# Performance work log

Measured on AMD Instinct MI355X. Metric: run time of the kernel, lower is better.

Reference implementation:

```python
import jax, jax.numpy as jnp
import numpy as np

B, N, D, H = 2, 192, 256, 8
DH = D // H
SCALE = 1.0 / float(np.sqrt(DH))


def setup_inputs() -> dict:
    key = jax.random.key(0)
    ks = jax.random.split(key, 20)
    def w(k, shape, s=0.02):
        return jax.random.normal(k, shape, dtype=jnp.float32) * s
    inp = {}
    inp['x'] = jax.random.normal(ks[0], (B, N, D), dtype=jnp.float32)
    inp['e'] = jax.random.normal(ks[1], (B, N, N, D), dtype=jnp.float32)
    for name in ['ln_x', 'ln_e', 'ln_x2', 'ln_e2']:
        inp[name + '_g'] = jnp.ones((D,), jnp.float32)
        inp[name + '_b'] = jnp.zeros((D,), jnp.float32)
    # per-head stacked projection weights: [H, D, DH]
    for i, n in enumerate(['Wq_en', 'Wk_en', 'Wv_en', 'Wq_ne', 'Wk_ne', 'Wv_ne']):
        inp[n] = w(ks[2 + i], (H, D, DH))
        inp['b' + n[1:]] = jnp.zeros((H, DH), jnp.float32)
    inp['WOx_w'] = w(ks[10], (D, D)); inp['WOx_b'] = jnp.zeros((D,), jnp.float32)
    inp['WOe_w'] = w(ks[11], (D, D)); inp['WOe_b'] = jnp.zeros((D,), jnp.float32)
    inp['mlpx_w1'] = w(ks[12], (4 * D, D)); inp['mlpx_b1'] = jnp.zeros((4 * D,), jnp.float32)
    inp['mlpx_w2'] = w(ks[13], (D, 4 * D)); inp['mlpx_b2'] = jnp.zeros((D,), jnp.float32)
    inp['mlpe_w1'] = w(ks[14], (4 * D, D)); inp['mlpe_b1'] = jnp.zeros((4 * D,), jnp.float32)
    inp['mlpe_w2'] = w(ks[15], (D, 4 * D)); inp['mlpe_b2'] = jnp.zeros((D,), jnp.float32)
    return inp


def layer_norm(v, g, b, eps=1e-5):
    m = jnp.mean(v, axis=-1, keepdims=True)
    var = jnp.mean((v - m) ** 2, axis=-1, keepdims=True)
    return (v - m) * jax.lax.rsqrt(var + eps) * g + b


def reference(x, e, ln_x_g, ln_x_b, ln_e_g, ln_e_b, ln_x2_g, ln_x2_b, ln_e2_g, ln_e2_b,
              Wq_en, bq_en, Wk_en, bk_en, Wv_en, bv_en,
              Wq_ne, bq_ne, Wk_ne, bk_ne, Wv_ne, bv_ne,
              WOx_w, WOx_b, WOe_w, WOe_b,
              mlpx_w1, mlpx_b1, mlpx_w2, mlpx_b2,
              mlpe_w1, mlpe_b1, mlpe_w2, mlpe_b2):
    b_, n_, d_ = x.shape
    xn = layer_norm(x, ln_x_g, ln_x_b)
    en = layer_norm(e, ln_e_g, ln_e_b)

    # --- edge-to-node cross attention (node i attends over its edges (i, j)) ---
    Q = jnp.einsum('bnd,hde->bnhe', xn, Wq_en) + bq_en          # [B,N,H,DH]
    K = jnp.einsum('bijd,hde->bijhe', en, Wk_en) + bk_en        # [B,N,N,H,DH]
    V = jnp.einsum('bijd,hde->bijhe', en, Wv_en) + bv_en
    s = jnp.einsum('bihe,bijhe->bijh', Q, K) * SCALE            # [B,N,N,H]
    a = jax.nn.softmax(s, axis=2)
    x_heads = jnp.einsum('bijh,bijhe->bihe', a, V)              # [B,N,H,DH]
    x_mha = x_heads.reshape(b_, n_, d_) @ WOx_w.T + WOx_b

    # --- node-to-edge cross attention (edge (i,j) attends over endpoints i, j) ---
    Qe = jnp.einsum('bijd,hde->bijhe', en, Wq_ne) + bq_ne       # [B,N,N,H,DH]
    Kx = jnp.einsum('bnd,hde->bnhe', xn, Wk_ne) + bk_ne         # [B,N,H,DH]
    Vx = jnp.einsum('bnd,hde->bnhe', xn, Wv_ne) + bv_ne
    si = jnp.einsum('bijhe,bihe->bijh', Qe, Kx) * SCALE
    sj = jnp.einsum('bijhe,bjhe->bijh', Qe, Kx) * SCALE
    m = jnp.maximum(si, sj)
    ei = jnp.exp(si - m)
    ej = jnp.exp(sj - m)
    den = ei + ej
    ai = (ei / den)[..., None]                                   # [B,N,N,H,1]
    aj = (ej / den)[..., None]
    e_heads = ai * Vx[:, :, None] + aj * Vx[:, None, :]          # [B,N,N,H,DH]
    e_mha = e_heads.reshape(b_, n_, n_, d_) @ WOe_w.T + WOe_b

    # --- residuals + MLPs ---
    x_out = xn + x_mha
    hx = layer_norm(x_out, ln_x2_g, ln_x2_b)
    hx = jax.nn.leaky_relu(hx @ mlpx_w1.T + mlpx_b1, 0.01) @ mlpx_w2.T + mlpx_b2
    x_out = x_out + hx

    e_out = en + e_mha
    he = layer_norm(e_out, ln_e2_g, ln_e2_b)
    he = jax.nn.leaky_relu(he @ mlpe_w1.T + mlpe_b1, 0.01) @ mlpe_w2.T + mlpe_b2
    e_out = e_out + he
    return (x_out, e_out)
```

## Files before the change

### kernel.cpp

```cpp
#include <hip/hip_runtime.h>
#include <hip/hip_bf16.h>
#include <math.h>

#define BB 2
#define NN 192
#define DD 256
#define HH 8
#define DHH 32
#define SCALE 0.17677669529663687f
#define SJ 4
#define NTILE (BB * NN * 6)

typedef __attribute__((ext_vector_type(8))) short short8;
typedef __attribute__((ext_vector_type(4))) float f32x4;


__device__ __forceinline__ float red32(float v) {
    v += __shfl_xor(v, 16);
    v += __shfl_xor(v, 8);
    v += __shfl_xor(v, 4);
    v += __shfl_xor(v, 2);
    v += __shfl_xor(v, 1);
    return v;
}

__device__ __forceinline__ unsigned short f2bf(float f) {
    unsigned int u = __builtin_bit_cast(unsigned int, f);
    u += 0x7FFFu + ((u >> 16) & 1u);
    return (unsigned short)(u >> 16);
}

__device__ __forceinline__ float bf2f(unsigned short u) {
    unsigned int v = ((unsigned int)u) << 16;
    return __builtin_bit_cast(float, v);
}

__device__ __forceinline__ void ln8(float (*xs)[DD], const float* __restrict__ g,
                                    const float* __restrict__ b,
                                    float* mred, float* rred) {
    int t = threadIdx.x;
    int r = t >> 5, l = t & 31;
    float s = 0.f, s2 = 0.f;
#pragma unroll
    for (int u = 0; u < 8; u++) {
        float v = xs[r][l + 32 * u];
        s += v; s2 += v * v;
    }
    s = red32(s); s2 = red32(s2);
    if (l == 0) {
        float mean = s * (1.f / 256.f);
        float var  = s2 * (1.f / 256.f) - mean * mean;
        mred[r] = mean;
        rred[r] = rsqrtf(var + 1e-5f);
    }
    __syncthreads();
    float gt = g[t], bt = b[t];
#pragma unroll
    for (int rr = 0; rr < 8; rr++) {
        float v = xs[rr][t];
        xs[rr][t] = (v - mred[rr]) * rred[rr] * gt + bt;
    }
    __syncthreads();
}

__device__ __forceinline__ void gemm256f8(const unsigned short (*A)[264],
                                          const unsigned short* __restrict__ Wf,
                                          int w, int lane, int fr, int fq,
                                          f32x4 acc[2][2]) {
#pragma unroll
    for (int m = 0; m < 2; m++)
#pragma unroll
        for (int nt = 0; nt < 2; nt++) acc[m][nt] = (f32x4){0.f, 0.f, 0.f, 0.f};
    short8 nb[2];
#pragma unroll
    for (int nt = 0; nt < 2; nt++)
        nb[nt] = *(const short8*)(Wf + (((size_t)(w * 2 + nt) * 8 + 0) * 64 + lane) * 8);
#pragma unroll
    for (int k = 0; k < 8; k++) {
        short8 cb[2];
#pragma unroll
        for (int nt = 0; nt < 2; nt++) cb[nt] = nb[nt];
        if (k < 7) {
#pragma unroll
            for (int nt = 0; nt < 2; nt++)
                nb[nt] = *(const short8*)(Wf + (((size_t)(w * 2 + nt) * 8 + k + 1) * 64 + lane) * 8);
        }
        short8 a0 = *(const short8*)&A[fr][k * 32 + fq * 8];
        short8 a1 = *(const short8*)&A[16 + fr][k * 32 + fq * 8];
#pragma unroll
        for (int nt = 0; nt < 2; nt++) {
            acc[0][nt] = __builtin_amdgcn_mfma_f32_16x16x32_bf16(a0, cb[nt], acc[0][nt], 0, 0, 0);
            acc[1][nt] = __builtin_amdgcn_mfma_f32_16x16x32_bf16(a1, cb[nt], acc[1][nt], 0, 0, 0);
        }
    }
}

__global__ void k_node_prep(const float* __restrict__ x,
                            const float* __restrict__ lnxg, const float* __restrict__ lnxb,
                            const float* __restrict__ Wq, const float* __restrict__ bq,
                            const float* __restrict__ Wk, const float* __restrict__ bk,
                            const float* __restrict__ Wv, const float* __restrict__ bv,
                            float* __restrict__ xn, float* __restrict__ Qb,
                            float* __restrict__ Kx, float* __restrict__ Vx) {
    __shared__ float xs[8][DD];
    __shared__ float mred[8], rred[8];
    int t = threadIdx.x;
    int r0 = blockIdx.x * 8;
    for (int r = 0; r < 8; r++) xs[r][t] = x[(r0 + r) * DD + t];
    __syncthreads();
    ln8(xs, lnxg, lnxb, mred, rred);
    for (int r = 0; r < 8; r++) xn[(r0 + r) * DD + t] = xs[r][t];
    int h = t >> 5, d_ = t & 31;
    const float* wq = Wq + h * DD * DHH + d_;
    const float* wk = Wk + h * DD * DHH + d_;
    const float* wv = Wv + h * DD * DHH + d_;
    float aq[8] = {0}, ak[8] = {0}, av[8] = {0};
    for (int k = 0; k < DD; k++) {
        float w1 = wq[k * DHH], w2 = wk[k * DHH], w3 = wv[k * DHH];
#pragma unroll
        for (int r = 0; r < 8; r++) {
            float e = xs[r][k];
            aq[r] += e * w1; ak[r] += e * w2; av[r] += e * w3;
        }
    }
    float bqt = bq[t], bkt = bk[t], bvt = bv[t];
    for (int r = 0; r < 8; r++) {
        Qb[(r0 + r) * DD + t] = aq[r] + bqt;
        Kx[(r0 + r) * DD + t] = ak[r] + bkt;
        Vx[(r0 + r) * DD + t] = av[r] + bvt;
    }
}

__global__ void k_cvt_all(const float* __restrict__ w1, const float* __restrict__ w2,
                          const float* __restrict__ WOe,
                          const float* __restrict__ Wq, const float* __restrict__ Wk,
                          const float* __restrict__ Wv,
                          unsigned short* __restrict__ w1f, unsigned short* __restrict__ w2f,
                          unsigned short* __restrict__ WOef,
                          unsigned short* __restrict__ Wqf, unsigned short* __restrict__ Wkf,
                          unsigned short* __restrict__ Wvf) {
    int bid = blockIdx.x, t = threadIdx.x;
    short8 out;
    if (bid < 128) {
        int fi = bid * 256 + t;
        int l = fi & 63, g = fi >> 6;
        int fr = l & 15, fq = l >> 4;
        int tau = g >> 3, kap = g & 7;
        const float* src = w1 + (size_t)(tau * 16 + fr) * 256 + kap * 32 + fq * 8;
#pragma unroll
        for (int u = 0; u < 8; u++) out[u] = (short)f2bf(src[u]);
        *(short8*)(w1f + (size_t)fi * 8) = out;
    } else if (bid < 256) {
        int fi = (bid - 128) * 256 + t;
        int l = fi & 63, g = fi >> 6;
        int fr = l & 15, fq = l >> 4;
        int tau = g >> 5, kap = g & 31;
        const float* src = w2 + (size_t)(tau * 16 + fr) * 1024 + kap * 32 + fq * 8;
#pragma unroll
        for (int u = 0; u < 8; u++) out[u] = (short)f2bf(src[u]);
        *(short8*)(w2f + (size_t)fi * 8) = out;
    } else if (bid < 288) {
        int fi = (bid - 256) * 256 + t;
        int l = fi & 63, g = fi >> 6;
        int fr = l & 15, fq = l >> 4;
        int tau = g >> 3, kap = g & 7;
        const float* src = WOe + (size_t)(tau * 16 + fr) * 256 + kap * 32 + fq * 8;
#pragma unroll
        for (int u = 0; u < 8; u++) out[u] = (short)f2bf(src[u]);
        *(short8*)(WOef + (size_t)fi * 8) = out;
    } else {
        int which = (bid - 288) >> 5;
        int fi = ((bid - 288) & 31) * 256 + t;
        int l = fi & 63, g = fi >> 6;
        int fr = l & 15, fq = l >> 4;
        int tau = g >> 3, kap = g & 7;
        int n = tau * 16 + fr;
        int k0 = kap * 32 + fq * 8;
        const float* src = which == 0 ? Wq : which == 1 ? Wk : Wv;
        const float* s2 = src + (size_t)(n >> 5) * 8192 + (n & 31);
#pragma unroll
        for (int u = 0; u < 8; u++) out[u] = (short)f2bf(s2[(size_t)(k0 + u) * 32]);
        unsigned short* dst = which == 0 ? Wqf : which == 1 ? Wkf : Wvf;
        *(short8*)(dst + (size_t)fi * 8) = out;
    }
}

__global__ __launch_bounds__(512, 2) void k_n2e_fused(
    const float* __restrict__ e,
    const float* __restrict__ lneg, const float* __restrict__ lneb,
    const unsigned short* __restrict__ Wqf, const float* __restrict__ bq,
    const unsigned short* __restrict__ Wkf, const float* __restrict__ bk,
    const unsigned short* __restrict__ Wvf, const float* __restrict__ bv,
    const float* __restrict__ Kx, const float* __restrict__ Vx,
    const unsigned short* __restrict__ WOef, const float* __restrict__ WOb,
    const float* __restrict__ ln2g, const float* __restrict__ ln2b,
    const unsigned short* __restrict__ w1f, const float* __restrict__ b1,
    const unsigned short* __restrict__ w2f, const float* __restrict__ b2,
    float* __restrict__ oute, unsigned short* __restrict__ Kb,
    unsigned short* __restrict__ Vb) {
    __shared__ unsigned short a_bf[32][264];
    __shared__ unsigned short p_bf[32][264];
    __shared__ float KxiS[DD], VxiS[DD];
    __shared__ float mrow[32], rrow[32];
    __shared__ float sW[32][8], s2W[32][8];
    __shared__ float m2s[32], r2s[32];
    int t = threadIdx.x, lane = t & 63, w = t >> 6;
    int fr = lane & 15, fq = lane >> 4;
    int blk = blockIdx.x;
    int b   = blk / (NN * 6);
    int rem = blk % (NN * 6);
    int i   = rem / 6;
    int j0  = (rem % 6) * 32;
    int node = b * NN + i;
    size_t ebase = ((size_t)node * NN + j0) * DD;

    {
        int r = t >> 4, sub = t & 15;
        const float4* src4 = (const float4*)(e + ebase + (size_t)r * DD + sub * 16);
        float vals[16];
        float s = 0.f, s2 = 0.f;
#pragma unroll
        for (int u = 0; u < 4; u++) {
            float4 v = src4[u];
            vals[4 * u + 0] = v.x; vals[4 * u + 1] = v.y;
            vals[4 * u + 2] = v.z; vals[4 * u + 3] = v.w;
            s += v.x + v.y + v.z + v.w;
            s2 += v.x * v.x + v.y * v.y + v.z * v.z + v.w * v.w;
        }
        s += __shfl_xor(s, 8); s2 += __shfl_xor(s2, 8);
        s += __shfl_xor(s, 4); s2 += __shfl_xor(s2, 4);
        s += __shfl_xor(s, 2); s2 += __shfl_xor(s2, 2);
        s += __shfl_xor(s, 1); s2 += __shfl_xor(s2, 1);
        float mean = s * (1.f / 256.f);
        float rstd = rsqrtf(s2 * (1.f / 256.f) - mean * mean + 1e-5f);
        if (sub == 0) { mrow[r] = mean; rrow[r] = rstd; }
#pragma unroll
        for (int u = 0; u < 16; u += 2) {
            int col = sub * 16 + u;
            float n0 = (vals[u]     - mean) * rstd * lneg[col]     + lneb[col];
            float n1 = (vals[u + 1] - mean) * rstd * lneg[col + 1] + lneb[col + 1];
            unsigned int pk = (unsigned int)f2bf(n0) | ((unsigned int)f2bf(n1) << 16);
            *(unsigned int*)&a_bf[r][col] = pk;
        }
    }
    if (t < DD) {
        KxiS[t] = Kx[node * DD + t];
        VxiS[t] = Vx[node * DD + t];
    }
    __syncthreads();

    const int nw = w * 32;

    f32x4 accQ[2][2];
    gemm256f8(a_bf, Wqf, w, lane, fr, fq, accQ);
    {
        float bqv[2];
#pragma unroll
        for (int nt = 0; nt < 2; nt++) bqv[nt] = bq[nw + nt * 16 + fr];
#pragma unroll
        for (int m = 0; m < 2; m++)
#pragma unroll
            for (int nt = 0; nt < 2; nt++)
#pragma unroll
                for (int j = 0; j < 4; j++) accQ[m][nt][j] += bqv[nt];
    }

    {
        f32x4 accK[2][2];
        gemm256f8(a_bf, Wkf, w, lane, fr, fq, accK);
#pragma unroll
        for (int nt = 0; nt < 2; nt++) {
            float bb = bk[nw + nt * 16 + fr];
#pragma unroll
            for (int m = 0; m < 2; m++)
#pragma unroll
                for (int j = 0; j < 4; j++)
                    p_bf[m * 16 + fq * 4 + j][nw + nt * 16 + fr] = f2bf(accK[m][nt][j] + bb);
        }
    }
    __syncthreads();
#pragma unroll
    for (int rp = 0; rp < 2; rp++) {
        int r = rp * 16 + (t >> 5);
        int c = (t & 31) * 8;
        short8 v = *(const short8*)&p_bf[r][c];
        *(short8*)(Kb + ebase + (size_t)r * DD + c) = v;
    }
    __syncthreads();

    {
        f32x4 accV[2][2];
        gemm256f8(a_bf, Wvf, w, lane, fr, fq, accV);
#pragma unroll
        for (int nt = 0; nt < 2; nt++) {
            float bb = bv[nw + nt * 16 + fr];
#pragma unroll
            for (int m = 0; m < 2; m++)
#pragma unroll
                for (int j = 0; j < 4; j++)
                    p_bf[m * 16 + fq * 4 + j][nw + nt * 16 + fr] = f2bf(accV[m][nt][j] + bb);
        }
    }
    __syncthreads();
#pragma unroll
    for (int rp = 0; rp < 2; rp++) {
        int r = rp * 16 + (t >> 5);
        int c = (t & 31) * 8;
        short8 v = *(const short8*)&p_bf[r][c];
        *(short8*)(Vb + ebase + (size_t)r * DD + c) = v;
    }
    __syncthreads();

    float KxiL[2], VxiL[2];
#pragma unroll
    for (int nt = 0; nt < 2; nt++) {
        KxiL[nt] = KxiS[nw + nt * 16 + fr];
        VxiL[nt] = VxiS[nw + nt * 16 + fr];
    }
    float ai[2][4], aj[2][4];
    {
        float Kxj[2][2][4];
#pragma unroll
        for (int m = 0; m < 2; m++)
#pragma unroll
            for (int nt = 0; nt < 2; nt++)
#pragma unroll
                for (int j = 0; j < 4; j++) {
                    int row = m * 16 + fq * 4 + j;
                    Kxj[m][nt][j] = Kx[(size_t)(b * NN + j0 + row) * DD + nw + nt * 16 + fr];
                }
#pragma unroll
        for (int m = 0; m < 2; m++)
#pragma unroll
            for (int j = 0; j < 4; j++) {
                float p = accQ[m][0][j] * KxiL[0] + accQ[m][1][j] * KxiL[1];
                float q = accQ[m][0][j] * Kxj[m][0][j] + accQ[m][1][j] * Kxj[m][1][j];
#pragma unroll
                for (int mk = 1; mk <= 8; mk <<= 1) {
                    p += __shfl_xor(p, mk);
                    q += __shfl_xor(q, mk);
                }
                p *= SCALE; q *= SCALE;
                float mx = fmaxf(p, q);
                float ei = __expf(p - mx), ej = __expf(q - mx);
                float inv = 1.f / (ei + ej);
                ai[m][j] = ei * inv; aj[m][j] = ej * inv;
            }
    }
    {
        float Vxj[2][2][4];
#pragma unroll
        for (int m = 0; m < 2; m++)
#pragma unroll
            for (int nt = 0; nt < 2; nt++)
#pragma unroll
                for (int j = 0; j < 4; j++) {
                    int row = m * 16 + fq * 4 + j;
                    Vxj[m][nt][j] = Vx[(size_t)(b * NN + j0 + row) * DD + nw + nt * 16 + fr];
                }
#pragma unroll
        for (int m = 0; m < 2; m++)
#pragma unroll
            for (int nt = 0; nt < 2; nt++)
#pragma unroll
                for (int j = 0; j < 4; j++) {
                    float v = ai[m][j] * VxiL[nt] + aj[m][j] * Vxj[m][nt][j];
                    p_bf[m * 16 + fq * 4 + j][nw + nt * 16 + fr] = f2bf(v);
                }
    }
    __syncthreads();

    f32x4 accO[2][2];
    gemm256f8(p_bf, WOef, w, lane, fr, fq, accO);

    float epre[2][2][4];
#pragma unroll
    for (int nt = 0; nt < 2; nt++) {
        int col = nw + nt * 16 + fr;
        float bo = WOb[col];
        float gc = lneg[col], bc = lneb[col];
#pragma unroll
        for (int m = 0; m < 2; m++)
#pragma unroll
            for (int j = 0; j < 4; j++) {
                int row = m * 16 + fq * 4 + j;
                float ev = e[ebase + (size_t)row * DD + col];
                float resid = (ev - mrow[row]) * rrow[row] * gc + bc;
                epre[m][nt][j] = resid + accO[m][nt][j] + bo;
            }
    }

#pragma unroll
    for (int m = 0; m < 2; m++)
#pragma unroll
        for (int j = 0; j < 4; j++) {
            float s  = epre[m][0][j] + epre[m][1][j];
            float s2 = epre[m][0][j] * epre[m][0][j] + epre[m][1][j] * epre[m][1][j];
#pragma unroll
            for (int mk = 1; mk <= 8; mk <<= 1) {
                s += __shfl_xor(s, mk);
                s2 += __shfl_xor(s2, mk);
            }
            if (fr == 0) {
                int row = m * 16 + fq * 4 + j;
                sW[row][w] = s;
                s2W[row][w] = s2;
            }
        }
    __syncthreads();
    if (t < 32) {
        float S = 0.f, S2 = 0.f;
#pragma unroll
        for (int ww = 0; ww < 8; ww++) { S += sW[t][ww]; S2 += s2W[t][ww]; }
        float mean = S * (1.f / 256.f);
        float var  = S2 * (1.f / 256.f) - mean * mean;
        m2s[t] = mean;
        r2s[t] = rsqrtf(var + 1e-5f);
    }
    __syncthreads();

#pragma unroll
    for (int nt = 0; nt < 2; nt++) {
        int col = nw + nt * 16 + fr;
        float g2 = ln2g[col], b2c = ln2b[col];
#pragma unroll
        for (int m = 0; m < 2; m++)
#pragma unroll
            for (int j = 0; j < 4; j++) {
                int row = m * 16 + fq * 4 + j;
                p_bf[row][col] = f2bf((epre[m][nt][j] - m2s[row]) * r2s[row] * g2 + b2c);
            }
    }
    __syncthreads();

#define B1ADDR(c, nt, k) (w1f + (((size_t)((c) * 16 + w * 2 + (nt)) * 8 + (k)) * 64 + lane) * 8)
#define B2ADDR(nt, c, k) (w2f + (((size_t)(w * 2 + (nt)) * 32 + (c) * 8 + (k)) * 64 + lane) * 8)
    f32x4 accM[2][2];
#pragma unroll
    for (int m = 0; m < 2; m++)
#pragma unroll
        for (int nt = 0; nt < 2; nt++) accM[m][nt] = (f32x4){0.f, 0.f, 0.f, 0.f};

    for (int c = 0; c < 4; c++) {
        f32x4 acc1[2][2];
#pragma unroll
        for (int m = 0; m < 2; m++)
#pragma unroll
            for (int nt = 0; nt < 2; nt++) acc1[m][nt] = (f32x4){0.f, 0.f, 0.f, 0.f};
        {
            short8 nb[2];
#pragma unroll
            for (int nt = 0; nt < 2; nt++) nb[nt] = *(const short8*)B1ADDR(c, nt, 0);
#pragma unroll
            for (int k = 0; k < 8; k++) {
                short8 cb[2];
#pragma unroll
                for (int nt = 0; nt < 2; nt++) cb[nt] = nb[nt];
                if (k < 7) {
#pragma unroll
                    for (int nt = 0; nt < 2; nt++) nb[nt] = *(const short8*)B1ADDR(c, nt, k + 1);
                }
                short8 a0 = *(const short8*)&p_bf[fr][k * 32 + fq * 8];
                short8 a1 = *(const short8*)&p_bf[16 + fr][k * 32 + fq * 8];
#pragma unroll
                for (int nt = 0; nt < 2; nt++) {
                    acc1[0][nt] = __builtin_amdgcn_mfma_f32_16x16x32_bf16(a0, cb[nt], acc1[0][nt], 0, 0, 0);
                    acc1[1][nt] = __builtin_amdgcn_mfma_f32_16x16x32_bf16(a1, cb[nt], acc1[1][nt], 0, 0, 0);
                }
            }
        }
#pragma unroll
        for (int nt = 0; nt < 2; nt++) {
            int ncol = nw + nt * 16 + fr;
            float bias = b1[c * 256 + ncol];
#pragma unroll
            for (int m = 0; m < 2; m++)
#pragma unroll
                for (int j = 0; j < 4; j++) {
                    float v = acc1[m][nt][j] + bias;
                    v = v > 0.f ? v : 0.01f * v;
                    a_bf[m * 16 + fq * 4 + j][ncol] = f2bf(v);
                }
        }
        __syncthreads();
        {
            short8 nb[2];
#pragma unroll
            for (int nt = 0; nt < 2; nt++) nb[nt] = *(const short8*)B2ADDR(nt, c, 0);
#pragma unroll
            for (int k = 0; k < 8; k++) {
                short8 cb[2];
#pragma unroll
                for (int nt = 0; nt < 2; nt++) cb[nt] = nb[nt];
                if (k < 7) {
#pragma unroll
                    for (int nt = 0; nt < 2; nt++) nb[nt] = *(const short8*)B2ADDR(nt, c, k + 1);
                }
                short8 h0 = *(const short8*)&a_bf[fr][k * 32 + fq * 8];
                short8 h1 = *(const short8*)&a_bf[16 + fr][k * 32 + fq * 8];
#pragma unroll
                for (int nt = 0; nt < 2; nt++) {
                    accM[0][nt] = __builtin_amdgcn_mfma_f32_16x16x32_bf16(h0, cb[nt], accM[0][nt], 0, 0, 0);
                    accM[1][nt] = __builtin_amdgcn_mfma_f32_16x16x32_bf16(h1, cb[nt], accM[1][nt], 0, 0, 0);
                }
            }
        }
        __syncthreads();
    }
#undef B1ADDR
#undef B2ADDR

#pragma unroll
    for (int nt = 0; nt < 2; nt++) {
        int col = nw + nt * 16 + fr;
        float bias = b2[col];
#pragma unroll
        for (int m = 0; m < 2; m++)
#pragma unroll
            for (int j = 0; j < 4; j++) {
                int row = m * 16 + fq * 4 + j;
                oute[ebase + (size_t)row * DD + col] = epre[m][nt][j] + accM[m][nt][j] + bias;
            }
    }
}

__global__ void k_e2n_lite(const unsigned short* __restrict__ Kb,
                           const unsigned short* __restrict__ Vb,
                           const float* __restrict__ Qb,
                           float* __restrict__ accP, float* __restrict__ mP,
                           float* __restrict__ lP) {
    __shared__ float accS[8][DD];
    __shared__ float mS[8][HH], lS[8][HH];
    int t = threadIdx.x;
    int s = blockIdx.x & (SJ - 1);
    int row = blockIdx.x >> 2;
    int g = t >> 5;
    int d0 = (t & 31) * 8;
    float qv[8];
    {
        const float4* q4 = (const float4*)(Qb + (size_t)row * DD + d0);
        float4 a = q4[0], b4 = q4[1];
        qv[0] = a.x; qv[1] = a.y; qv[2] = a.z; qv[3] = a.w;
        qv[4] = b4.x; qv[5] = b4.y; qv[6] = b4.z; qv[7] = b4.w;
    }
    float m_s = -1e30f, l_s = 0.f;
    float acc[8];
#pragma unroll
    for (int u = 0; u < 8; u++) acc[u] = 0.f;
    size_t base = (size_t)row * NN * DD;
    for (int it = 0; it < NN / SJ / 8; it++) {
        int j = s * (NN / SJ) + it * 8 + g;
        short8 kv = *(const short8*)(Kb + base + (size_t)j * DD + d0);
        short8 vv = *(const short8*)(Vb + base + (size_t)j * DD + d0);
        float part = 0.f;
#pragma unroll
        for (int u = 0; u < 8; u++) part += qv[u] * bf2f((unsigned short)kv[u]);
        part += __shfl_xor(part, 1);
        part += __shfl_xor(part, 2);
        float sc = part * SCALE;
        float mn = fmaxf(m_s, sc);
        float c = __expf(m_s - mn);
        float p = __expf(sc - mn);
        l_s = l_s * c + p;
#pragma unroll
        for (int u = 0; u < 8; u++) acc[u] = acc[u] * c + p * bf2f((unsigned short)vv[u]);
        m_s = mn;
    }
#pragma unroll
    for (int u = 0; u < 8; u++) accS[g][d0 + u] = acc[u];
    if ((t & 3) == 0) {
        int h = (t & 31) >> 2;
        mS[g][h] = m_s;
        lS[g][h] = l_s;
    }
    __syncthreads();
    int H = t >> 5;
    float mm = -1e30f;
#pragma unroll
    for (int g2 = 0; g2 < 8; g2++) mm = fmaxf(mm, mS[g2][H]);
    float ll = 0.f, aa = 0.f;
#pragma unroll
    for (int g2 = 0; g2 < 8; g2++) {
        float c = __expf(mS[g2][H] - mm);
        ll += lS[g2][H] * c;
        aa += accS[g2][t] * c;
    }
    accP[((size_t)s * BB * NN + row) * DD + t] = aa;
    if ((t & 31) == 0) {
        mP[(s * BB * NN + row) * HH + H] = mm;
        lP[(s * BB * NN + row) * HH + H] = ll;
    }
}

__global__ void k_e2n_merge(const float* __restrict__ accP, const float* __restrict__ mP,
                            const float* __restrict__ lP, float* __restrict__ xh) {
    int t = threadIdx.x, row = blockIdx.x, h = t >> 5;
    float m = -1e30f;
    for (int s = 0; s < SJ; s++) m = fmaxf(m, mP[(s * BB * NN + row) * HH + h]);
    float num = 0.f, den = 0.f;
    for (int s = 0; s < SJ; s++) {
        float c = __expf(mP[(s * BB * NN + row) * HH + h] - m);
        num += accP[((size_t)s * BB * NN + row) * DD + t] * c;
        den += lP[(s * BB * NN + row) * HH + h] * c;
    }
    xh[row * DD + t] = num / den;
}

__global__ void k_x_epi(const float* __restrict__ xh, const float* __restrict__ xn,
                        const float* __restrict__ WO, const float* __restrict__ WOb,
                        const float* __restrict__ ln2g, const float* __restrict__ ln2b,
                        const float* __restrict__ w1, const float* __restrict__ b1,
                        const float* __restrict__ w2, const float* __restrict__ b2,
                        float* __restrict__ outx) {
    __shared__ float hsrc[8][DD];
    __shared__ float xs[8][DD];
    __shared__ float ls[8][DD];
    __shared__ float hh[8][1024];
    __shared__ float mred[8], rred[8];
    int t = threadIdx.x;
    int r0 = blockIdx.x * 8;
    for (int r = 0; r < 8; r++) hsrc[r][t] = xh[(r0 + r) * DD + t];
    __syncthreads();
    float acc[8] = {0};
    const float* wrow = WO + (size_t)t * DD;
    for (int k = 0; k < DD; k++) {
        float w = wrow[k];
#pragma unroll
        for (int r = 0; r < 8; r++) acc[r] += hsrc[r][k] * w;
    }
    float wob = WOb[t];
    for (int r = 0; r < 8; r++) {
        float v = xn[(r0 + r) * DD + t] + acc[r] + wob;
        xs[r][t] = v;
        ls[r][t] = v;
    }
    __syncthreads();
    ln8(ls, ln2g, ln2b, mred, rred);
    for (int p = 0; p < 4; p++) {
        int q = t + p * 256;
        float a2[8] = {0};
        const float* w1r = w1 + (size_t)q * DD;
        for (int k = 0; k < DD; k++) {
            float w = w1r[k];
#pragma unroll
            for (int r = 0; r < 8; r++) a2[r] += ls[r][k] * w;
        }
        float b1q = b1[q];
        for (int r = 0; r < 8; r++) {
            float v = a2[r] + b1q;
            hh[r][q] = v > 0.f ? v : 0.01f * v;
        }
    }
    __syncthreads();
    float a3[8] = {0};
    const float* w2r = w2 + (size_t)t * 1024;
    for (int q = 0; q < 1024; q++) {
        float w = w2r[q];
#pragma unroll
        for (int r = 0; r < 8; r++) a3[r] += hh[r][q] * w;
    }
    float b2t = b2[t];
    for (int r = 0; r < 8; r++)
        outx[(r0 + r) * DD + t] = xs[r][t] + a3[r] + b2t;
}

__global__ void k_e2n_attn(const float* __restrict__ e,
                           const float* __restrict__ lneg, const float* __restrict__ lneb,
                           const float* __restrict__ Wk, const float* __restrict__ bk,
                           const float* __restrict__ Wv, const float* __restrict__ bv,
                           const float* __restrict__ Qb,
                           float* __restrict__ accP, float* __restrict__ mP,
                           float* __restrict__ lP) {
    __shared__ float es[8][DD];
    __shared__ float mred[8], rred[8];
    int t = threadIdx.x;
    int s = blockIdx.x & (SJ - 1);
    int row = blockIdx.x >> 2;
    int h = t >> 5, d_ = t & 31;
    float qt = Qb[row * DD + t];
    float m_s = -1e30f, l_s = 0.f, acc = 0.f;
    const float* wk = Wk + h * DD * DHH + d_;
    const float* wv = Wv + h * DD * DHH + d_;
    float bkt = bk[t], bvt = bv[t];
    for (int j0 = s * (NN / SJ); j0 < (s + 1) * (NN / SJ); j0 += 8) {
        for (int r = 0; r < 8; r++)
            es[r][t] = e[((size_t)row * NN + j0 + r) * DD + t];
        __syncthreads();
        ln8(es, lneg, lneb, mred, rred);
        float aK[8] = {0}, aV[8] = {0};
        for (int k = 0; k < DD; k++) {
            float w1 = wk[k * DHH], w2 = wv[k * DHH];
#pragma unroll
            for (int r = 0; r < 8; r++) {
                float ev = es[r][k];
                aK[r] += ev * w1; aV[r] += ev * w2;
            }
        }
#pragma unroll
        for (int r = 0; r < 8; r++) {
            float sc = red32(qt * (aK[r] + bkt)) * SCALE;
            float vn = aV[r] + bvt;
            float mn = fmaxf(m_s, sc);
            float c = __expf(m_s - mn);
            float p = __expf(sc - mn);
            l_s = l_s * c + p;
            acc = acc * c + p * vn;
            m_s = mn;
        }
        __syncthreads();
    }
    accP[((size_t)s * BB * NN + row) * DD + t] = acc;
    if (d_ == 0) {
        mP[(s * BB * NN + row) * HH + h] = m_s;
        lP[(s * BB * NN + row) * HH + h] = l_s;
    }
}

__global__ void k_n2e(const float* __restrict__ e,
                      const float* __restrict__ lneg, const float* __restrict__ lneb,
                      const float* __restrict__ Wq, const float* __restrict__ bq,
                      const float* __restrict__ Kx, const float* __restrict__ Vx,
                      const float* __restrict__ WO, const float* __restrict__ WOb,
                      float* __restrict__ oute) {
    __shared__ float es[8][DD];
    __shared__ float hs[8][DD];
    __shared__ float mred[8], rred[8];
    int t = threadIdx.x, h = t >> 5, d_ = t & 31;
    int blk = blockIdx.x;
    int b = blk / (NN * (NN / 8));
    int rem = blk % (NN * (NN / 8));
    int i = rem / (NN / 8);
    int j0 = (rem % (NN / 8)) * 8;
    size_t ebase = ((size_t)(b * NN + i) * NN + j0) * DD;
    for (int r = 0; r < 8; r++) es[r][t] = e[ebase + (size_t)r * DD + t];
    __syncthreads();
    ln8(es, lneg, lneb, mred, rred);
    float aQ[8] = {0};
    const float* wq = Wq + h * DD * DHH + d_;
    for (int k = 0; k < DD; k++) {
        float w = wq[k * DHH];
#pragma unroll
        for (int r = 0; r < 8; r++) aQ[r] += es[r][k] * w;
    }
    float bqt = bq[t];
    float kxi = Kx[(b * NN + i) * DD + t];
    float vxi = Vx[(b * NN + i) * DD + t];
#pragma unroll
    for (int r = 0; r < 8; r++) {
        float qe = aQ[r] + bqt;
        float si = red32(qe * kxi) * SCALE;
        float kxj = Kx[(b * NN + j0 + r) * DD + t];
        float sj = red32(qe * kxj) * SCALE;
        float mx = fmaxf(si, sj);
        float ei = __expf(si - mx), ej = __expf(sj - mx);
        float inv = 1.f / (ei + ej);
        float vxj = Vx[(b * NN + j0 + r) * DD + t];
        hs[r][t] = (ei * inv) * vxi + (ej * inv) * vxj;
    }
    __syncthreads();
    float aO[8] = {0};
    const float* wrow = WO + (size_t)t * DD;
    for (int k = 0; k < DD; k++) {
        float w = wrow[k];
#pragma unroll
        for (int r = 0; r < 8; r++) aO[r] += hs[r][k] * w;
    }
    float wob = WOb[t];
    for (int r = 0; r < 8; r++)
        oute[ebase + (size_t)r * DD + t] = es[r][t] + aO[r] + wob;
}

__global__ void k_cvt_w_fb(const float* __restrict__ w1, const float* __restrict__ w2,
                           unsigned short* __restrict__ w1b, unsigned short* __restrict__ w2b) {
    int i = blockIdx.x * 256 + threadIdx.x;
    w1b[i] = f2bf(w1[i]);
    w2b[i] = f2bf(w2[i]);
}

__global__ void k_e_mlp_f32(float* __restrict__ oute,
                            const float* __restrict__ ln2g, const float* __restrict__ ln2b,
                            const float* __restrict__ w1, const float* __restrict__ b1,
                            const float* __restrict__ w2, const float* __restrict__ b2) {
    __shared__ float xs[8][DD];
    __shared__ float ls[8][DD];
    __shared__ float hh[8][1024];
    __shared__ float mred[8], rred[8];
    int t = threadIdx.x;
    size_t r0 = (size_t)blockIdx.x * 8;
    for (int r = 0; r < 8; r++) {
        float v = oute[(r0 + r) * DD + t];
        xs[r][t] = v;
        ls[r][t] = v;
    }
    __syncthreads();
    ln8(ls, ln2g, ln2b, mred, rred);
    for (int p = 0; p < 4; p++) {
        int q = t + p * 256;
        float a2[8] = {0};
        const float* w1r = w1 + (size_t)q * DD;
        for (int k = 0; k < DD; k++) {
            float w = w1r[k];
#pragma unroll
            for (int r = 0; r < 8; r++) a2[r] += ls[r][k] * w;
        }
        float b1q = b1[q];
        for (int r = 0; r < 8; r++) {
            float v = a2[r] + b1q;
            hh[r][q] = v > 0.f ? v : 0.01f * v;
        }
    }
    __syncthreads();
    float a3[8] = {0};
    const float* w2r = w2 + (size_t)t * 1024;
    for (int q = 0; q < 1024; q++) {
        float w = w2r[q];
#pragma unroll
        for (int r = 0; r < 8; r++) a3[r] += hh[r][q] * w;
    }
    float b2t = b2[t];
    for (int r = 0; r < 8; r++)
        oute[(r0 + r) * DD + t] = xs[r][t] + a3[r] + b2t;
}

extern "C" void kernel_launch(void* const* d_in, const int* in_sizes, int n_in,
                              void* d_out, int out_size, void* d_ws, size_t ws_size,
                              hipStream_t stream) {
    (void)in_sizes; (void)n_in; (void)out_size;
    const float* x      = (const float*)d_in[0];
    const float* e      = (const float*)d_in[1];
    const float* ln_x_g = (const float*)d_in[2];
    const float* ln_x_b = (const float*)d_in[3];
    const float* ln_e_g = (const float*)d_in[4];
    const float* ln_e_b = (const float*)d_in[5];
    const float* ln_x2_g = (const float*)d_in[6];
    const float* ln_x2_b = (const float*)d_in[7];
    const float* ln_e2_g = (const float*)d_in[8];
    const float* ln_e2_b = (const float*)d_in[9];
    const float* Wq_en = (const float*)d_in[10];
    const float* bq_en = (const float*)d_in[11];
    const float* Wk_en = (const float*)d_in[12];
    const float* bk_en = (const float*)d_in[13];
    const float* Wv_en = (const float*)d_in[14];
    const float* bv_en = (const float*)d_in[15];
    const float* Wq_ne = (const float*)d_in[16];
    const float* bq_ne = (const float*)d_in[17];
    const float* Wk_ne = (const float*)d_in[18];
    const float* bk_ne = (const float*)d_in[19];
    const float* Wv_ne = (const float*)d_in[20];
    const float* bv_ne = (const float*)d_in[21];
    const float* WOx_w = (const float*)d_in[22];
    const float* WOx_b = (const float*)d_in[23];
    const float* WOe_w = (const float*)d_in[24];
    const float* WOe_b = (const float*)d_in[25];
    const float* mlpx_w1 = (const float*)d_in[26];
    const float* mlpx_b1 = (const float*)d_in[27];
    const float* mlpx_w2 = (const float*)d_in[28];
    const float* mlpx_b2 = (const float*)d_in[29];
    const float* mlpe_w1 = (const float*)d_in[30];
    const float* mlpe_b1 = (const float*)d_in[31];
    const float* mlpe_w2 = (const float*)d_in[32];
    const float* mlpe_b2 = (const float*)d_in[33];

    float* out_x = (float*)d_out;
    float* out_e = out_x + (size_t)BB * NN * DD;

    float* ws = (float*)d_ws;
    float* xn   = ws;
    float* Qb   = xn + 98304;
    float* Kx   = Qb + 98304;
    float* Vx   = Kx + 98304;
    float* xh   = Vx + 98304;
    float* accP = xh + 98304;
    float* mP   = accP + 393216;
    float* lP   = mP + 12288;
    unsigned short* w1f  = (unsigned short*)(lP + 12288);
    unsigned short* w2f  = w1f + 262144;
    unsigned short* WOef = w2f + 262144;
    unsigned short* Wqf  = WOef + 65536;
    unsigned short* Wkf  = Wqf + 65536;
    unsigned short* Wvf  = Wkf + 65536;
    unsigned short* Kb   = Wvf + 65536;
    unsigned short* Vb   = Kb + 18874368;

    const size_t NEED = 909312ull * 4 + 38453504ull * 2;
    bool mfma_path = ws_size >= NEED;

    dim3 blk(256);

    k_node_prep<<<dim3(BB * NN / 8), blk, 0, stream>>>(
        x, ln_x_g, ln_x_b, Wq_en, bq_en, Wk_ne, bk_ne, Wv_ne, bv_ne,
        xn, Qb, Kx, Vx);

    if (mfma_path) {
        k_cvt_all<<<dim3(384), blk, 0, stream>>>(
            mlpe_w1, mlpe_w2, WOe_w, Wq_ne, Wk_en, Wv_en,
            w1f, w2f, WOef, Wqf, Wkf, Wvf);

        k_n2e_fused<<<dim3(NTILE), dim3(512), 0, stream>>>(
            e, ln_e_g, ln_e_b, Wqf, bq_ne, Wkf, bk_en, Wvf, bv_en,
            Kx, Vx, WOef, WOe_b,
            ln_e2_g, ln_e2_b, w1f, mlpe_b1, w2f, mlpe_b2,
            out_e, Kb, Vb);

        k_e2n_lite<<<dim3(BB * NN * SJ), blk, 0, stream>>>(
            Kb, Vb, Qb, accP, mP, lP);

        k_e2n_merge<<<dim3(BB * NN), blk, 0, stream>>>(accP, mP, lP, xh);

        k_x_epi<<<dim3(BB * NN / 8), blk, 0, stream>>>(
            xh, xn, WOx_w, WOx_b, ln_x2_g, ln_x2_b,
            mlpx_w1, mlpx_b1, mlpx_w2, mlpx_b2, out_x);
    } else {
        k_n2e<<<dim3(BB * NN * (NN / 8)), blk, 0, stream>>>(
            e, ln_e_g, ln_e_b, Wq_ne, bq_ne, Kx, Vx, WOe_w, WOe_b, out_e);

        k_e2n_attn<<<dim3(BB * NN * SJ), blk, 0, stream>>>(
            e, ln_e_g, ln_e_b, Wk_en, bk_en, Wv_en, bv_en, Qb, accP, mP, lP);

        k_e2n_merge<<<dim3(BB * NN), blk, 0, stream>>>(accP, mP, lP, xh);

        k_x_epi<<<dim3(BB * NN / 8), blk, 0, stream>>>(
            xh, xn, WOx_w, WOx_b, ln_x2_g, ln_x2_b,
            mlpx_w1, mlpx_b1, mlpx_w2, mlpx_b2, out_x);

        k_e_mlp_f32<<<dim3(BB * NN * NN / 8), blk, 0, stream>>>(
            out_e, ln_e2_g, ln_e2_b, mlpe_w1, mlpe_b1, mlpe_w2, mlpe_b2);
    }
}
```

Baseline: 475.4 us.

## Deepen weight prefetch to two stages and write K/V straight to global

The weight-fragment register prefetch in the MFMA GEMM loops (the shared gemm256f8 and both MLP GEMMs) now runs two k-steps ahead instead of one, to hide more global/L2 load latency behind the MFMAs. The K and V projection outputs are now written directly from accumulator registers to global memory as scattered 2-byte stores. This removes the LDS staging and four __syncthreads barriers. The trade-off is more vector registers for the deeper prefetch, which may lower occupancy, and uncoalesced narrow global stores in place of 16-byte coalesced ones.

Result: slower. 487.1 us (+2.5%).

```diff
diff --git a/kernel.cpp b/kernel.cpp
--- a/kernel.cpp
+++ b/kernel.cpp
@@ -71,19 +71,21 @@
     for (int m = 0; m < 2; m++)
 #pragma unroll
         for (int nt = 0; nt < 2; nt++) acc[m][nt] = (f32x4){0.f, 0.f, 0.f, 0.f};
-    short8 nb[2];
-#pragma unroll
-    for (int nt = 0; nt < 2; nt++)
-        nb[nt] = *(const short8*)(Wf + (((size_t)(w * 2 + nt) * 8 + 0) * 64 + lane) * 8);
+    short8 q0[2], q1[2];
+#pragma unroll
+    for (int nt = 0; nt < 2; nt++) {
+        q0[nt] = *(const short8*)(Wf + (((size_t)(w * 2 + nt) * 8 + 0) * 64 + lane) * 8);
+        q1[nt] = *(const short8*)(Wf + (((size_t)(w * 2 + nt) * 8 + 1) * 64 + lane) * 8);
+    }
 #pragma unroll
     for (int k = 0; k < 8; k++) {
         short8 cb[2];
 #pragma unroll
-        for (int nt = 0; nt < 2; nt++) cb[nt] = nb[nt];
-        if (k < 7) {
+        for (int nt = 0; nt < 2; nt++) { cb[nt] = q0[nt]; q0[nt] = q1[nt]; }
+        if (k < 6) {
 #pragma unroll
             for (int nt = 0; nt < 2; nt++)
-                nb[nt] = *(const short8*)(Wf + (((size_t)(w * 2 + nt) * 8 + k + 1) * 64 + lane) * 8);
+                q1[nt] = *(const short8*)(Wf + (((size_t)(w * 2 + nt) * 8 + k + 2) * 64 + lane) * 8);
         }
         short8 a0 = *(const short8*)&A[fr][k * 32 + fq * 8];
         short8 a1 = *(const short8*)&A[16 + fr][k * 32 + fq * 8];
@@ -270,46 +272,34 @@
         gemm256f8(a_bf, Wkf, w, lane, fr, fq, accK);
 #pragma unroll
         for (int nt = 0; nt < 2; nt++) {
-            float bb = bk[nw + nt * 16 + fr];
+            int col = nw + nt * 16 + fr;
+            float bb = bk[col];
 #pragma unroll
             for (int m = 0; m < 2; m++)
 #pragma unroll
-                for (int j = 0; j < 4; j++)
-                    p_bf[m * 16 + fq * 4 + j][nw + nt * 16 + fr] = f2bf(accK[m][nt][j] + bb);
-        }
-    }
-    __syncthreads();
-#pragma unroll
-    for (int rp = 0; rp < 2; rp++) {
-        int r = rp * 16 + (t >> 5);
-        int c = (t & 31) * 8;
-        short8 v = *(const short8*)&p_bf[r][c];
-        *(short8*)(Kb + ebase + (size_t)r * DD + c) = v;
-    }
-    __syncthreads();
+                for (int j = 0; j < 4; j++) {
+                    int row = m * 16 + fq * 4 + j;
+                    Kb[ebase + (size_t)row * DD + col] = f2bf(accK[m][nt][j] + bb);
+                }
+        }
+    }
 
     {
         f32x4 accV[2][2];
         gemm256f8(a_bf, Wvf, w, lane, fr, fq, accV);
 #pragma unroll
         for (int nt = 0; nt < 2; nt++) {
-            float bb = bv[nw + nt * 16 + fr];
+            int col = nw + nt * 16 + fr;
+            float bb = bv[col];
 #pragma unroll
             for (int m = 0; m < 2; m++)
 #pragma unroll
-                for (int j = 0; j < 4; j++)
-                    p_bf[m * 16 + fq * 4 + j][nw + nt * 16 + fr] = f2bf(accV[m][nt][j] + bb);
-        }
-    }
-    __syncthreads();
-#pragma unroll
-    for (int rp = 0; rp < 2; rp++) {
-        int r = rp * 16 + (t >> 5);
-        int c = (t & 31) * 8;
-        short8 v = *(const short8*)&p_bf[r][c];
-        *(short8*)(Vb + ebase + (size_t)r * DD + c) = v;
-    }
-    __syncthreads();
+                for (int j = 0; j < 4; j++) {
+                    int row = m * 16 + fq * 4 + j;
+                    Vb[ebase + (size_t)row * DD + col] = f2bf(accV[m][nt][j] + bb);
+                }
+        }
+    }
 
     float KxiL[2], VxiL[2];
 #pragma unroll
@@ -448,17 +438,20 @@
 #pragma unroll
             for (int nt = 0; nt < 2; nt++) acc1[m][nt] = (f32x4){0.f, 0.f, 0.f, 0.f};
         {
-            short8 nb[2];
-#pragma unroll
-            for (int nt = 0; nt < 2; nt++) nb[nt] = *(const short8*)B1ADDR(c, nt, 0);
+            short8 q0[2], q1[2];
+#pragma unroll
+            for (int nt = 0; nt < 2; nt++) {
+                q0[nt] = *(const short8*)B1ADDR(c, nt, 0);
+                q1[nt] = *(const short8*)B1ADDR(c, nt, 1);
+            }
 #pragma unroll
             for (int k = 0; k < 8; k++) {
                 short8 cb[2];
 #pragma unroll
-                for (int nt = 0; nt < 2; nt++) cb[nt] = nb[nt];
-                if (k < 7) {
-#pragma unroll
-                    for (int nt = 0; nt < 2; nt++) nb[nt] = *(const short8*)B1ADDR(c, nt, k + 1);
+                for (int nt = 0; nt < 2; nt++) { cb[nt] = q0[nt]; q0[nt] = q1[nt]; }
+                if (k < 6) {
+#pragma unroll
+                    for (int nt = 0; nt < 2; nt++) q1[nt] = *(const short8*)B1ADDR(c, nt, k + 2);
                 }
                 short8 a0 = *(const short8*)&p_bf[fr][k * 32 + fq * 8];
                 short8 a1 = *(const short8*)&p_bf[16 + fr][k * 32 + fq * 8];
@@ -484,17 +477,20 @@
         }
         __syncthreads();
         {
-            short8 nb[2];
-#pragma unroll
-            for (int nt = 0; nt < 2; nt++) nb[nt] = *(const short8*)B2ADDR(nt, c, 0);
+            short8 q0[2], q1[2];
+#pragma unroll
+            for (int nt = 0; nt < 2; nt++) {
+                q0[nt] = *(const short8*)B2ADDR(nt, c, 0);
+                q1[nt] = *(const short8*)B2ADDR(nt, c, 1);
+            }
 #pragma unroll
             for (int k = 0; k < 8; k++) {
                 short8 cb[2];
 #pragma unroll
-                for (int nt = 0; nt < 2; nt++) cb[nt] = nb[nt];
-                if (k < 7) {
-#pragma unroll
-                    for (int nt = 0; nt < 2; nt++) nb[nt] = *(const short8*)B2ADDR(nt, c, k + 1);
+                for (int nt = 0; nt < 2; nt++) { cb[nt] = q0[nt]; q0[nt] = q1[nt]; }
+                if (k < 6) {
+#pragma unroll
+                    for (int nt = 0; nt < 2; nt++) q1[nt] = *(const short8*)B2ADDR(nt, c, k + 2);
                 }
                 short8 h0 = *(const short8*)&a_bf[fr][k * 32 + fq * 8];
                 short8 h1 = *(const short8*)&a_bf[16 + fr][k * 32 + fq * 8];
```

## Fuse edge-to-node attention into n2e kernel, drop K/V bf16 round-trip

Applied to the files above, without the earlier changes.

Computes edge-to-node attention scores and the softmax-weighted V partial sums directly from the K and V MFMA accumulators inside the fused edge kernel. Each 32-edge tile writes per-head max, sum and partial accumulators for 6 splits, which a generalized merge kernel combines. This removes writing and re-reading the large bf16 K and V tensors (about 75 MB) and one kernel launch. In exchange it adds more registers and shuffle reductions in an already heavy kernel, which may lower occupancy.

Result: faster. 422.6 us (-11.1%).

```diff
diff --git a/kernel.cpp b/kernel.cpp
--- a/kernel.cpp
+++ b/kernel.cpp
@@ -9,6 +9,7 @@
 #define DHH 32
 #define SCALE 0.17677669529663687f
 #define SJ 4
+#define NS6 6
 #define NTILE (BB * NN * 6)
 
 typedef __attribute__((ext_vector_type(8))) short short8;
@@ -192,15 +193,16 @@
     const unsigned short* __restrict__ Wkf, const float* __restrict__ bk,
     const unsigned short* __restrict__ Wvf, const float* __restrict__ bv,
     const float* __restrict__ Kx, const float* __restrict__ Vx,
+    const float* __restrict__ Qb,
     const unsigned short* __restrict__ WOef, const float* __restrict__ WOb,
     const float* __restrict__ ln2g, const float* __restrict__ ln2b,
     const unsigned short* __restrict__ w1f, const float* __restrict__ b1,
     const unsigned short* __restrict__ w2f, const float* __restrict__ b2,
-    float* __restrict__ oute, unsigned short* __restrict__ Kb,
-    unsigned short* __restrict__ Vb) {
+    float* __restrict__ oute,
+    float* __restrict__ accP6, float* __restrict__ mP6, float* __restrict__ lP6) {
     __shared__ unsigned short a_bf[32][264];
     __shared__ unsigned short p_bf[32][264];
-    __shared__ float KxiS[DD], VxiS[DD];
+    __shared__ float KxiS[DD], VxiS[DD], QbS[DD];
     __shared__ float mrow[32], rrow[32];
     __shared__ float sW[32][8], s2W[32][8];
     __shared__ float m2s[32], r2s[32];
@@ -210,7 +212,8 @@
     int b   = blk / (NN * 6);
     int rem = blk % (NN * 6);
     int i   = rem / 6;
-    int j0  = (rem % 6) * 32;
+    int spl = rem % 6;
+    int j0  = spl * 32;
     int node = b * NN + i;
     size_t ebase = ((size_t)node * NN + j0) * DD;
 
@@ -246,6 +249,7 @@
     if (t < DD) {
         KxiS[t] = Kx[node * DD + t];
         VxiS[t] = Vx[node * DD + t];
+        QbS[t]  = Qb[node * DD + t];
     }
     __syncthreads();
 
@@ -265,51 +269,82 @@
                 for (int j = 0; j < 4; j++) accQ[m][nt][j] += bqv[nt];
     }
 
+    f32x4 accK[2][2];
+    gemm256f8(a_bf, Wkf, w, lane, fr, fq, accK);
+#pragma unroll
+    for (int nt = 0; nt < 2; nt++) {
+        float bb = bk[nw + nt * 16 + fr];
+#pragma unroll
+        for (int m = 0; m < 2; m++)
+#pragma unroll
+            for (int j = 0; j < 4; j++) accK[m][nt][j] += bb;
+    }
+
+    f32x4 accV[2][2];
+    gemm256f8(a_bf, Wvf, w, lane, fr, fq, accV);
+#pragma unroll
+    for (int nt = 0; nt < 2; nt++) {
+        float bb = bv[nw + nt * 16 + fr];
+#pragma unroll
+        for (int m = 0; m < 2; m++)
+#pragma unroll
+            for (int j = 0; j < 4; j++) accV[m][nt][j] += bb;
+    }
+
     {
-        f32x4 accK[2][2];
-        gemm256f8(a_bf, Wkf, w, lane, fr, fq, accK);
+        float QbL[2];
+        QbL[0] = QbS[nw + fr];
+        QbL[1] = QbS[nw + 16 + fr];
+        float p[2][4];
+        float mx = -1e30f;
+#pragma unroll
+        for (int m = 0; m < 2; m++)
+#pragma unroll
+            for (int j = 0; j < 4; j++) {
+                float s = accK[m][0][j] * QbL[0] + accK[m][1][j] * QbL[1];
+                s += __shfl_xor(s, 1);
+                s += __shfl_xor(s, 2);
+                s += __shfl_xor(s, 4);
+                s += __shfl_xor(s, 8);
+                s *= SCALE;
+                p[m][j] = s;
+                mx = fmaxf(mx, s);
+            }
+        mx = fmaxf(mx, __shfl_xor(mx, 16));
+        mx = fmaxf(mx, __shfl_xor(mx, 32));
+        float lsum = 0.f;
+#pragma unroll
+        for (int m = 0; m < 2; m++)
+#pragma unroll
+            for (int j = 0; j < 4; j++) {
+                p[m][j] = __expf(p[m][j] - mx);
+                lsum += p[m][j];
+            }
+        lsum += __shfl_xor(lsum, 16);
+        lsum += __shfl_xor(lsum, 32);
+        float part[2];
 #pragma unroll
         for (int nt = 0; nt < 2; nt++) {
-            float bb = bk[nw + nt * 16 + fr];
+            float acc = 0.f;
 #pragma unroll
             for (int m = 0; m < 2; m++)
 #pragma unroll
                 for (int j = 0; j < 4; j++)
-                    p_bf[m * 16 + fq * 4 + j][nw + nt * 16 + fr] = f2bf(accK[m][nt][j] + bb);
-        }
-    }
-    __syncthreads();
-#pragma unroll
-    for (int rp = 0; rp < 2; rp++) {
-        int r = rp * 16 + (t >> 5);
-        int c = (t & 31) * 8;
-        short8 v = *(const short8*)&p_bf[r][c];
-        *(short8*)(Kb + ebase + (size_t)r * DD + c) = v;
-    }
-    __syncthreads();
-
-    {
-        f32x4 accV[2][2];
-        gemm256f8(a_bf, Wvf, w, lane, fr, fq, accV);
-#pragma unroll
-        for (int nt = 0; nt < 2; nt++) {
-            float bb = bv[nw + nt * 16 + fr];
-#pragma unroll
-            for (int m = 0; m < 2; m++)
-#pragma unroll
-                for (int j = 0; j < 4; j++)
-                    p_bf[m * 16 + fq * 4 + j][nw + nt * 16 + fr] = f2bf(accV[m][nt][j] + bb);
-        }
-    }
-    __syncthreads();
-#pragma unroll
-    for (int rp = 0; rp < 2; rp++) {
-        int r = rp * 16 + (t >> 5);
-        int c = (t & 31) * 8;
-        short8 v = *(const short8*)&p_bf[r][c];
-        *(short8*)(Vb + ebase + (size_t)r * DD + c) = v;
-    }
-    __syncthreads();
+                    acc += p[m][j] * accV[m][nt][j];
+            acc += __shfl_xor(acc, 16);
+            acc += __shfl_xor(acc, 32);
+            part[nt] = acc;
+        }
+        if (fq == 0) {
+#pragma unroll
+            for (int nt = 0; nt < 2; nt++)
+                accP6[((size_t)spl * BB * NN + node) * DD + nw + nt * 16 + fr] = part[nt];
+            if (fr == 0) {
+                mP6[((size_t)spl * BB * NN + node) * HH + w] = mx;
+                lP6[((size_t)spl * BB * NN + node) * HH + w] = lsum;
+            }
+        }
+    }
 
     float KxiL[2], VxiL[2];
 #pragma unroll
@@ -524,81 +559,14 @@
     }
 }
 
-__global__ void k_e2n_lite(const unsigned short* __restrict__ Kb,
-                           const unsigned short* __restrict__ Vb,
-                           const float* __restrict__ Qb,
-                           float* __restrict__ accP, float* __restrict__ mP,
-                           float* __restrict__ lP) {
-    __shared__ float accS[8][DD];
-    __shared__ float mS[8][HH], lS[8][HH];
-    int t = threadIdx.x;
-    int s = blockIdx.x & (SJ - 1);
-    int row = blockIdx.x >> 2;
-    int g = t >> 5;
-    int d0 = (t & 31) * 8;
-    float qv[8];
-    {
-        const float4* q4 = (const float4*)(Qb + (size_t)row * DD + d0);
-        float4 a = q4[0], b4 = q4[1];
-        qv[0] = a.x; qv[1] = a.y; qv[2] = a.z; qv[3] = a.w;
-        qv[4] = b4.x; qv[5] = b4.y; qv[6] = b4.z; qv[7] = b4.w;
-    }
-    float m_s = -1e30f, l_s = 0.f;
-    float acc[8];
-#pragma unroll
-    for (int u = 0; u < 8; u++) acc[u] = 0.f;
-    size_t base = (size_t)row * NN * DD;
-    for (int it = 0; it < NN / SJ / 8; it++) {
-        int j = s * (NN / SJ) + it * 8 + g;
-        short8 kv = *(const short8*)(Kb + base + (size_t)j * DD + d0);
-        short8 vv = *(const short8*)(Vb + base + (size_t)j * DD + d0);
-        float part = 0.f;
-#pragma unroll
-        for (int u = 0; u < 8; u++) part += qv[u] * bf2f((unsigned short)kv[u]);
-        part += __shfl_xor(part, 1);
-        part += __shfl_xor(part, 2);
-        float sc = part * SCALE;
-        float mn = fmaxf(m_s, sc);
-        float c = __expf(m_s - mn);
-        float p = __expf(sc - mn);
-        l_s = l_s * c + p;
-#pragma unroll
-        for (int u = 0; u < 8; u++) acc[u] = acc[u] * c + p * bf2f((unsigned short)vv[u]);
-        m_s = mn;
-    }
-#pragma unroll
-    for (int u = 0; u < 8; u++) accS[g][d0 + u] = acc[u];
-    if ((t & 3) == 0) {
-        int h = (t & 31) >> 2;
-        mS[g][h] = m_s;
-        lS[g][h] = l_s;
-    }
-    __syncthreads();
-    int H = t >> 5;
-    float mm = -1e30f;
-#pragma unroll
-    for (int g2 = 0; g2 < 8; g2++) mm = fmaxf(mm, mS[g2][H]);
-    float ll = 0.f, aa = 0.f;
-#pragma unroll
-    for (int g2 = 0; g2 < 8; g2++) {
-        float c = __expf(mS[g2][H] - mm);
-        ll += lS[g2][H] * c;
-        aa += accS[g2][t] * c;
-    }
-    accP[((size_t)s * BB * NN + row) * DD + t] = aa;
-    if ((t & 31) == 0) {
-        mP[(s * BB * NN + row) * HH + H] = mm;
-        lP[(s * BB * NN + row) * HH + H] = ll;
-    }
-}
-
-__global__ void k_e2n_merge(const float* __restrict__ accP, const float* __restrict__ mP,
-                            const float* __restrict__ lP, float* __restrict__ xh) {
+__global__ void k_e2n_mergeN(const float* __restrict__ accP, const float* __restrict__ mP,
+                             const float* __restrict__ lP, float* __restrict__ xh,
+                             int nsplit) {
     int t = threadIdx.x, row = blockIdx.x, h = t >> 5;
     float m = -1e30f;
-    for (int s = 0; s < SJ; s++) m = fmaxf(m, mP[(s * BB * NN + row) * HH + h]);
+    for (int s = 0; s < nsplit; s++) m = fmaxf(m, mP[(s * BB * NN + row) * HH + h]);
     float num = 0.f, den = 0.f;
-    for (int s = 0; s < SJ; s++) {
+    for (int s = 0; s < nsplit; s++) {
         float c = __expf(mP[(s * BB * NN + row) * HH + h] - m);
         num += accP[((size_t)s * BB * NN + row) * DD + t] * c;
         den += lP[(s * BB * NN + row) * HH + h] * c;
@@ -768,13 +736,6 @@
     float wob = WOb[t];
     for (int r = 0; r < 8; r++)
         oute[ebase + (size_t)r * DD + t] = es[r][t] + aO[r] + wob;
-}
-
-__global__ void k_cvt_w_fb(const float* __restrict__ w1, const float* __restrict__ w2,
-                           unsigned short* __restrict__ w1b, unsigned short* __restrict__ w2b) {
-    int i = blockIdx.x * 256 + threadIdx.x;
-    w1b[i] = f2bf(w1[i]);
-    w2b[i] = f2bf(w2[i]);
 }
 
 __global__ void k_e_mlp_f32(float* __restrict__ oute,
@@ -879,8 +840,9 @@
     unsigned short* Wqf  = WOef + 65536;
     unsigned short* Wkf  = Wqf + 65536;
     unsigned short* Wvf  = Wkf + 65536;
-    unsigned short* Kb   = Wvf + 65536;
-    unsigned short* Vb   = Kb + 18874368;
+    float* accP6 = (float*)(Wvf + 65536);
+    float* mP6   = accP6 + 589824;
+    float* lP6   = mP6 + 18432;
 
     const size_t NEED = 909312ull * 4 + 38453504ull * 2;
     bool mfma_path = ws_size >= NEED;
@@ -898,14 +860,11 @@
 
         k_n2e_fused<<<dim3(NTILE), dim3(512), 0, stream>>>(
             e, ln_e_g, ln_e_b, Wqf, bq_ne, Wkf, bk_en, Wvf, bv_en,
-            Kx, Vx, WOef, WOe_b,
+            Kx, Vx, Qb, WOef, WOe_b,
             ln_e2_g, ln_e2_b, w1f, mlpe_b1, w2f, mlpe_b2,
-            out_e, Kb, Vb);
-
-        k_e2n_lite<<<dim3(BB * NN * SJ), blk, 0, stream>>>(
-            Kb, Vb, Qb, accP, mP, lP);
-
-        k_e2n_merge<<<dim3(BB * NN), blk, 0, stream>>>(accP, mP, lP, xh);
+            out_e, accP6, mP6, lP6);
+
+        k_e2n_mergeN<<<dim3(BB * NN), blk, 0, stream>>>(accP6, mP6, lP6, xh, NS6);
 
         k_x_epi<<<dim3(BB * NN / 8), blk, 0, stream>>>(
             xh, xn, WOx_w, WOx_b, ln_x2_g, ln_x2_b,
@@ -917,7 +876,7 @@
         k_e2n_attn<<<dim3(BB * NN * SJ), blk, 0, stream>>>(
             e, ln_e_g, ln_e_b, Wk_en, bk_en, Wv_en, bv_en, Qb, accP, mP, lP);
 
-        k_e2n_merge<<<dim3(BB * NN), blk, 0, stream>>>(accP, mP, lP, xh);
+        k_e2n_mergeN<<<dim3(BB * NN), blk, 0, stream>>>(accP, mP, lP, xh, SJ);
 
         k_x_epi<<<dim3(BB * NN / 8), blk, 0, stream>>>(
             xh, xn, WOx_w, WOx_b, ln_x2_g, ln_x2_b,
```
